# Performance work log

Hardware: AMD Instinct MI355X
Metric: run time of the kernel (lower is better)

## Reference

```python
import jax, jax.numpy as jnp
import numpy as np

B, T, D, H = 64, 512, 256, 512

def setup_inputs() -> dict:
    key = jax.random.key(0)
    ks = jax.random.split(key, 5)
    s = 1.0 / np.sqrt(D + H)  # keep gate pre-activations in a sane range
    return {
        "x": jax.random.normal(ks[0], (B, T, D), dtype=jnp.float32),
        "Wf": jax.random.normal(ks[1], (D + H, H), dtype=jnp.float32) * s,
        "bf": jnp.zeros((H,), dtype=jnp.float32),
        "Wi": jax.random.normal(ks[2], (D + H, H), dtype=jnp.float32) * s,
        "bi": jnp.zeros((H,), dtype=jnp.float32),
        "Wo": jax.random.normal(ks[3], (D + H, H), dtype=jnp.float32) * s,
        "bo": jnp.zeros((H,), dtype=jnp.float32),
        "Wc": jax.random.normal(ks[4], (D + H, H), dtype=jnp.float32) * s,
        "bc": jnp.zeros((H,), dtype=jnp.float32),
    }

def reference(x, Wf, bf, Wi, bi, Wo, bo, Wc, bc):
    # x: [B, T, D]; unidirectional LSTM, zero initial hidden/cell state.
    batch, dur, _ = x.shape
    hid = Wf.shape[1]
    h0 = jnp.zeros((batch, hid), dtype=x.dtype)
    c0 = jnp.zeros((batch, hid), dtype=x.dtype)

    def step(carry, xt):
        h, c = carry
        z = jnp.concatenate([xt, h], axis=1)  # [B, D+H]
        f = jax.nn.sigmoid(z @ Wf + bf)
        i = jax.nn.sigmoid(z @ Wi + bi)
        c_tilde = jnp.tanh(z @ Wc + bc)
        o = jax.nn.sigmoid(z @ Wo + bo)
        c_new = c * f + c_tilde * i
        h_new = o * jnp.tanh(c_new)
        return (h_new, c_new), h_new

    _, hs = jax.lax.scan(step, (h0, c0), jnp.swapaxes(x, 0, 1))  # hs: [T, B, H]
    return jnp.swapaxes(hs, 0, 1)  # [B, T, H]
```

## Files before the change

### kernel.cpp

```cpp
#include <hip/hip_runtime.h>


#define T_   512
#define D_   256
#define H_   512
#define NCL  4
#define WPC  32
#define BPC  16
#define NKT  24
#define ZW   768

typedef __attribute__((ext_vector_type(8)))  short  short8;
typedef __attribute__((ext_vector_type(4)))  float  f32x4;
typedef __attribute__((ext_vector_type(4)))  float  float4_;
typedef unsigned short ushort_t;
typedef unsigned int   uint_t;

__device__ __forceinline__ ushort_t f2bf(float f) {
    unsigned int u = __float_as_uint(f);
    u += 0x7FFFu + ((u >> 16) & 1u);
    return (ushort_t)(u >> 16);
}
__device__ __forceinline__ float sigm_(float x) { return 1.0f / (1.0f + __expf(-x)); }
__device__ __forceinline__ float tanh_(float x) {
    float a = fabsf(x);
    float e = __expf(-2.0f * a);
    float r = (1.0f - e) / (1.0f + e);
    return copysignf(r, x);
}


__device__ __forceinline__ void zbuild_x1(ushort_t* zbuf, int bx, int ch,
                                          float4_ xr0, float4_ xr1,
                                          float4_ xr2, float4_ xr3)
{
    short8 a0, a1;
#pragma unroll
    for (int e = 0; e < 4; ++e) {
        a0[e]     = (short)f2bf(xr0[e]);
        a0[4 + e] = (short)f2bf(xr1[e]);
        a1[e]     = (short)f2bf(xr2[e]);
        a1[4 + e] = (short)f2bf(xr3[e]);
    }
    const int s = bx & 7;
    *(short8*)(zbuf + bx * ZW + (((ch * 2    ) ^ s) << 3)) = a0;
    *(short8*)(zbuf + bx * ZW + (((ch * 2 + 1) ^ s) << 3)) = a1;
}

__global__ __launch_bounds__(256, 1)
void lstm_persistent(const float* __restrict__ x,
                     const float* __restrict__ Wf, const float* __restrict__ bf_,
                     const float* __restrict__ Wi, const float* __restrict__ bi_,
                     const float* __restrict__ Wo, const float* __restrict__ bo_,
                     const float* __restrict__ Wc, const float* __restrict__ bc_,
                     float* __restrict__ out,
                     uint_t* __restrict__ flags,
                     uint_t* __restrict__ hexch)
{
    __shared__ ushort_t w_lds[4 * NKT * 512];
    __shared__ ushort_t z2[2][16 * ZW];
    __shared__ float    gate_lds[4][16][20];
    __shared__ float    bias_lds[64];

    const int tid  = threadIdx.x;
    const int lane = tid & 63;
    const int wv   = tid >> 6;
    const int cl   = blockIdx.x >> 5;
    const int w    = blockIdx.x & 31;
    const int b0   = cl * BPC;
    const int hc0  = w * 16;

    for (int idx = tid; idx < 4 * NKT * 64; idx += 256) {
        int blk   = idx >> 6;
        int ln    = idx & 63;
        int ct    = blk / NKT;
        int kt    = blk % NKT;
        int j     = ct * 16 + (ln & 15);
        int hc    = j >> 2, g = j & 3;
        int gcol  = hc0 + hc;
        const float* Wsrc = (g == 0) ? Wf : ((g == 1) ? Wi : ((g == 2) ? Wo : Wc));
        int krow0 = kt * 32 + (ln >> 4) * 8;
        short8 v;
#pragma unroll
        for (int jj = 0; jj < 8; ++jj)
            v[jj] = (short)f2bf(Wsrc[(size_t)(krow0 + jj) * H_ + gcol]);
        *(short8*)(w_lds + blk * 512 + ln * 8) = v;
    }
    if (tid < 64) {
        int g = tid & 3, hc = tid >> 2;
        const float* bsrc = (g == 0) ? bf_ : ((g == 1) ? bi_ : ((g == 2) ? bo_ : bc_));
        bias_lds[tid] = bsrc[hc0 + hc];
    }

    const int bx = tid & 15, ch = tid >> 4;
    const int l15 = lane & 15, lk = lane >> 4;
    const int hidx = hc0 + wv * 4 + lk;
    const float* xbase = x + (size_t)(b0 + bx) * (T_ * D_) + ch * 16;

    float4_ xr0, xr1, xr2, xr3;
    {
        const float4_* p = (const float4_*)xbase;
        xr0 = p[0]; xr1 = p[1]; xr2 = p[2]; xr3 = p[3];
    }
    zbuild_x1(z2[0], bx, ch, xr0, xr1, xr2, xr3);
    {
        const int zblk0 = 32 + (tid >> 2), zoff2 = (tid & 3) * 2;
#pragma unroll
        for (int r = 0; r < 16; ++r)
            *(uint_t*)(z2[0] + r * ZW + ((zblk0 ^ (r & 7)) << 3) + zoff2) = 0u;
    }
    __syncthreads();

    short8 Bf[NKT];
#pragma unroll
    for (int kt = 0; kt < NKT; ++kt)
        Bf[kt] = *(const short8*)(w_lds + (wv * NKT + kt) * 512 + lane * 8);
    asm volatile("" ::: "memory");

    uint_t* flags_cl = flags + cl * WPC;
    uint_t* hex0 = hexch + ((size_t)0 * NCL + cl) * (BPC * 256);
    uint_t* hex1 = hexch + ((size_t)1 * NCL + cl) * (BPC * 256);

    float c_reg = 0.0f;
    const int s7 = l15 & 7;
    const int blk0 = 32 + (tid >> 2), off2 = (tid & 3) * 2;
    const size_t po = (size_t)l15 * 256 + (hidx >> 1);

    for (int t = 0; t < T_; ++t) {
        const ushort_t* zr = z2[t & 1] + l15 * ZW;
        f32x4 ac0 = {0.f,0.f,0.f,0.f}, ac1 = {0.f,0.f,0.f,0.f};
        f32x4 ac2 = {0.f,0.f,0.f,0.f}, ac3 = {0.f,0.f,0.f,0.f};
#pragma unroll
        for (int kt = 0; kt < NKT; kt += 4) {
            short8 a0 = *(const short8*)(zr + ((((kt + 0) * 4 + lk) ^ s7) << 3));
            short8 a1 = *(const short8*)(zr + ((((kt + 1) * 4 + lk) ^ s7) << 3));
            short8 a2 = *(const short8*)(zr + ((((kt + 2) * 4 + lk) ^ s7) << 3));
            short8 a3 = *(const short8*)(zr + ((((kt + 3) * 4 + lk) ^ s7) << 3));
            ac0 = __builtin_amdgcn_mfma_f32_16x16x32_bf16(a0, Bf[kt + 0], ac0, 0, 0, 0);
            ac1 = __builtin_amdgcn_mfma_f32_16x16x32_bf16(a1, Bf[kt + 1], ac1, 0, 0, 0);
            ac2 = __builtin_amdgcn_mfma_f32_16x16x32_bf16(a2, Bf[kt + 2], ac2, 0, 0, 0);
            ac3 = __builtin_amdgcn_mfma_f32_16x16x32_bf16(a3, Bf[kt + 3], ac3, 0, 0, 0);
        }
        f32x4 acc = (ac0 + ac1) + (ac2 + ac3);

        *(f32x4*)&gate_lds[wv][l15][lk * 4] = acc;
        asm volatile("s_waitcnt lgkmcnt(0)" ::: "memory");
        __builtin_amdgcn_sched_barrier(0);

        float pre[4];
#pragma unroll
        for (int g = 0; g < 4; ++g)
            pre[g] = bias_lds[(wv * 4 + lk) * 4 + g] + gate_lds[wv][lk * 4 + g][l15];

        float fg = sigm_(pre[0]);
        float ig = sigm_(pre[1]);
        float og = sigm_(pre[2]);
        float cc = tanh_(pre[3]);
        c_reg = fmaf(c_reg, fg, cc * ig);
        float hout = og * tanh_(c_reg);

        float hpart = __shfl_xor(hout, 16);
        if (!(lk & 1)) {
            uint_t pk = ((uint_t)f2bf(hpart) << 16) | (uint_t)f2bf(hout);
            uint_t* hp = (((t + 1) & 1) ? hex1 : hex0) + po;
            __hip_atomic_store(hp, pk, __ATOMIC_RELAXED, __HIP_MEMORY_SCOPE_AGENT);
        }

        asm volatile("s_waitcnt vmcnt(0)" ::: "memory");
        __builtin_amdgcn_sched_barrier(0);
        __syncthreads();
        if (tid == 0)
            __hip_atomic_store(flags_cl + w, (uint_t)(t + 1),
                               __ATOMIC_RELAXED, __HIP_MEMORY_SCOPE_AGENT);

        out[((size_t)(b0 + l15) * T_ + t) * H_ + hidx] = hout;
        if (t + 1 < T_) {
            const float4_* p = (const float4_*)(xbase + (size_t)(t + 1) * D_);
            xr0 = p[0]; xr1 = p[1]; xr2 = p[2]; xr3 = p[3];
        }

        if (t + 1 < T_) {
            ushort_t* zn = z2[(t + 1) & 1];

            if (lane < WPC) {
                const uint_t* fp = flags_cl + lane;
                while (__hip_atomic_load(fp, __ATOMIC_RELAXED,
                                         __HIP_MEMORY_SCOPE_AGENT) <= (uint_t)t)
                    __builtin_amdgcn_s_sleep(1);
            }

            const uint_t* hs = (((t + 1) & 1) ? hex1 : hex0);
            uint_t hv[16];
#pragma unroll
            for (int q = 0; q < 16; ++q)
                hv[q] = __hip_atomic_load(hs + q * 256 + tid,
                                          __ATOMIC_RELAXED, __HIP_MEMORY_SCOPE_AGENT);
#pragma unroll
            for (int q = 0; q < 16; ++q)
                *(uint_t*)(zn + q * ZW + ((blk0 ^ (q & 7)) << 3) + off2) = hv[q];

            zbuild_x1(zn, bx, ch, xr0, xr1, xr2, xr3);
        }

        __syncthreads();
    }
}

extern "C" void kernel_launch(void* const* d_in, const int* in_sizes, int n_in,
                              void* d_out, int out_size, void* d_ws, size_t ws_size,
                              hipStream_t stream) {
    const float* x  = (const float*)d_in[0];
    const float* Wf = (const float*)d_in[1];
    const float* bf = (const float*)d_in[2];
    const float* Wi = (const float*)d_in[3];
    const float* bi = (const float*)d_in[4];
    const float* Wo = (const float*)d_in[5];
    const float* bo = (const float*)d_in[6];
    const float* Wc = (const float*)d_in[7];
    const float* bc = (const float*)d_in[8];
    float* out = (float*)d_out;

    uint_t* flags = (uint_t*)d_ws;
    uint_t* hexch = (uint_t*)((char*)d_ws + 4096);

    hipMemsetAsync(d_ws, 0, 4096, stream);

    lstm_persistent<<<dim3(NCL * WPC), dim3(256), 0, stream>>>(
        x, Wf, bf, Wi, bi, Wo, bo, Wc, bc, out, flags, hexch);
}
```

Before: 1.553 ms.

## Regroup LSTM workgroups into 8 clusters of 8 batches with 32 hidden units each

```diff
diff --git a/kernel.cpp b/kernel.cpp
--- a/kernel.cpp
+++ b/kernel.cpp
@@ -4,9 +4,9 @@
 #define T_   512
 #define D_   256
 #define H_   512
-#define NCL  4
-#define WPC  32
-#define BPC  16
+#define NCL  8
+#define WPC  16
+#define BPC  8
 #define NKT  24
 #define ZW   768
 
@@ -29,23 +29,6 @@
     return copysignf(r, x);
 }
 
-
-__device__ __forceinline__ void zbuild_x1(ushort_t* zbuf, int bx, int ch,
-                                          float4_ xr0, float4_ xr1,
-                                          float4_ xr2, float4_ xr3)
-{
-    short8 a0, a1;
-#pragma unroll
-    for (int e = 0; e < 4; ++e) {
-        a0[e]     = (short)f2bf(xr0[e]);
-        a0[4 + e] = (short)f2bf(xr1[e]);
-        a1[e]     = (short)f2bf(xr2[e]);
-        a1[4 + e] = (short)f2bf(xr3[e]);
-    }
-    const int s = bx & 7;
-    *(short8*)(zbuf + bx * ZW + (((ch * 2    ) ^ s) << 3)) = a0;
-    *(short8*)(zbuf + bx * ZW + (((ch * 2 + 1) ^ s) << 3)) = a1;
-}
 
 __global__ __launch_bounds__(256, 1)
 void lstm_persistent(const float* __restrict__ x,
@@ -59,63 +42,79 @@
 {
     __shared__ ushort_t w_lds[4 * NKT * 512];
     __shared__ ushort_t z2[2][16 * ZW];
-    __shared__ float    gate_lds[4][16][20];
-    __shared__ float    bias_lds[64];
+    __shared__ float    gate_lds[4][2][16][12];
+    __shared__ float    bias_lds[128];
 
     const int tid  = threadIdx.x;
     const int lane = tid & 63;
     const int wv   = tid >> 6;
-    const int cl   = blockIdx.x >> 5;
-    const int w    = blockIdx.x & 31;
+    const int cl   = blockIdx.x >> 4;
+    const int w    = blockIdx.x & 15;
     const int b0   = cl * BPC;
-    const int hc0  = w * 16;
-
-    for (int idx = tid; idx < 4 * NKT * 64; idx += 256) {
-        int blk   = idx >> 6;
-        int ln    = idx & 63;
-        int ct    = blk / NKT;
-        int kt    = blk % NKT;
-        int j     = ct * 16 + (ln & 15);
-        int hc    = j >> 2, g = j & 3;
-        int gcol  = hc0 + hc;
-        const float* Wsrc = (g == 0) ? Wf : ((g == 1) ? Wi : ((g == 2) ? Wo : Wc));
-        int krow0 = kt * 32 + (ln >> 4) * 8;
-        short8 v;
-#pragma unroll
-        for (int jj = 0; jj < 8; ++jj)
-            v[jj] = (short)f2bf(Wsrc[(size_t)(krow0 + jj) * H_ + gcol]);
-        *(short8*)(w_lds + blk * 512 + ln * 8) = v;
-    }
-    if (tid < 64) {
+    const int hc0  = w * 32;
+
+    {
+        uint_t* zz = (uint_t*)z2;
+        for (int i = tid; i < 2 * 16 * ZW / 2; i += 256) zz[i] = 0;
+    }
+
+#define REPACK(CT_BASE)                                                        \
+    for (int idx = tid; idx < 4 * NKT * 64; idx += 256) {                      \
+        int blk   = idx >> 6;                                       \
+        int ln    = idx & 63;                                                  \
+        int ct    = (CT_BASE) + blk / NKT;                                     \
+        int kt    = blk % NKT;                                                 \
+        int j     = ct * 16 + (ln & 15);                  \
+        int hc    = j >> 2, g = j & 3;                                         \
+        int gcol  = hc0 + hc;                                                  \
+        const float* Wsrc = (g == 0) ? Wf : ((g == 1) ? Wi                     \
+                            : ((g == 2) ? Wo : Wc));                           \
+        int krow0 = kt * 32 + (ln >> 4) * 8;                                   \
+        short8 v;                                                              \
+        _Pragma("unroll")                                                      \
+        for (int jj = 0; jj < 8; ++jj)                                         \
+            v[jj] = (short)f2bf(Wsrc[(size_t)(krow0 + jj) * H_ + gcol]);       \
+        *(short8*)(w_lds + blk * 512 + ln * 8) = v;                            \
+    }
+    REPACK(4)
+    __syncthreads();
+
+    short8 Bf[NKT];
+#pragma unroll
+    for (int kt = 0; kt < NKT; ++kt)
+        Bf[kt] = *(const short8*)(w_lds + (wv * NKT + kt) * 512 + lane * 8);
+    asm volatile("" ::: "memory");
+    __syncthreads();
+
+    REPACK(0)
+#undef REPACK
+    if (tid < 128) {
         int g = tid & 3, hc = tid >> 2;
         const float* bsrc = (g == 0) ? bf_ : ((g == 1) ? bi_ : ((g == 2) ? bo_ : bc_));
         bias_lds[tid] = bsrc[hc0 + hc];
     }
 
-    const int bx = tid & 15, ch = tid >> 4;
+    const int bx = tid & 7, ch = tid >> 3;
     const int l15 = lane & 15, lk = lane >> 4;
-    const int hidx = hc0 + wv * 4 + lk;
-    const float* xbase = x + (size_t)(b0 + bx) * (T_ * D_) + ch * 16;
-
-    float4_ xr0, xr1, xr2, xr3;
+    const int gb   = lane >> 3;
+    const int hsel = lane & 7;
+    const int hcl  = (hsel < 4) ? (wv * 4 + hsel) : (16 + wv * 4 + (hsel - 4));
+    const int gtile = hsel >> 2;
+    const int gcol4 = (hsel & 3) * 4;
+    const float* xbase = x + (size_t)(b0 + bx) * (T_ * D_) + ch * 8;
+
     {
         const float4_* p = (const float4_*)xbase;
-        xr0 = p[0]; xr1 = p[1]; xr2 = p[2]; xr3 = p[3];
-    }
-    zbuild_x1(z2[0], bx, ch, xr0, xr1, xr2, xr3);
-    {
-        const int zblk0 = 32 + (tid >> 2), zoff2 = (tid & 3) * 2;
-#pragma unroll
-        for (int r = 0; r < 16; ++r)
-            *(uint_t*)(z2[0] + r * ZW + ((zblk0 ^ (r & 7)) << 3) + zoff2) = 0u;
+        float4_ x0 = p[0], x1 = p[1];
+        short8 a;
+#pragma unroll
+        for (int e = 0; e < 4; ++e) {
+            a[e]     = (short)f2bf(x0[e]);
+            a[4 + e] = (short)f2bf(x1[e]);
+        }
+        *(short8*)(z2[0] + bx * ZW + ((ch ^ (bx & 7)) << 3)) = a;
     }
     __syncthreads();
-
-    short8 Bf[NKT];
-#pragma unroll
-    for (int kt = 0; kt < NKT; ++kt)
-        Bf[kt] = *(const short8*)(w_lds + (wv * NKT + kt) * 512 + lane * 8);
-    asm volatile("" ::: "memory");
 
     uint_t* flags_cl = flags + cl * WPC;
     uint_t* hex0 = hexch + ((size_t)0 * NCL + cl) * (BPC * 256);
@@ -124,33 +123,39 @@
     float c_reg = 0.0f;
     const int s7 = l15 & 7;
     const int blk0 = 32 + (tid >> 2), off2 = (tid & 3) * 2;
-    const size_t po = (size_t)l15 * 256 + (hidx >> 1);
+    const size_t po = (size_t)gb * 256 + ((hc0 + hcl) >> 1);
+    const ushort_t* wl = w_lds + (wv * NKT) * 512 + lane * 8;
+    float4_ xq0, xq1;
 
     for (int t = 0; t < T_; ++t) {
         const ushort_t* zr = z2[t & 1] + l15 * ZW;
-        f32x4 ac0 = {0.f,0.f,0.f,0.f}, ac1 = {0.f,0.f,0.f,0.f};
-        f32x4 ac2 = {0.f,0.f,0.f,0.f}, ac3 = {0.f,0.f,0.f,0.f};
-#pragma unroll
-        for (int kt = 0; kt < NKT; kt += 4) {
-            short8 a0 = *(const short8*)(zr + ((((kt + 0) * 4 + lk) ^ s7) << 3));
-            short8 a1 = *(const short8*)(zr + ((((kt + 1) * 4 + lk) ^ s7) << 3));
-            short8 a2 = *(const short8*)(zr + ((((kt + 2) * 4 + lk) ^ s7) << 3));
-            short8 a3 = *(const short8*)(zr + ((((kt + 3) * 4 + lk) ^ s7) << 3));
-            ac0 = __builtin_amdgcn_mfma_f32_16x16x32_bf16(a0, Bf[kt + 0], ac0, 0, 0, 0);
-            ac1 = __builtin_amdgcn_mfma_f32_16x16x32_bf16(a1, Bf[kt + 1], ac1, 0, 0, 0);
-            ac2 = __builtin_amdgcn_mfma_f32_16x16x32_bf16(a2, Bf[kt + 2], ac2, 0, 0, 0);
-            ac3 = __builtin_amdgcn_mfma_f32_16x16x32_bf16(a3, Bf[kt + 3], ac3, 0, 0, 0);
-        }
-        f32x4 acc = (ac0 + ac1) + (ac2 + ac3);
-
-        *(f32x4*)&gate_lds[wv][l15][lk * 4] = acc;
+        f32x4 aL0 = {0.f,0.f,0.f,0.f}, aL1 = {0.f,0.f,0.f,0.f};
+        f32x4 aV0 = {0.f,0.f,0.f,0.f}, aV1 = {0.f,0.f,0.f,0.f};
+#pragma unroll
+        for (int kt = 0; kt < NKT; kt += 2) {
+            short8 a0  = *(const short8*)(zr + ((((kt + 0) * 4 + lk) ^ s7) << 3));
+            short8 a1  = *(const short8*)(zr + ((((kt + 1) * 4 + lk) ^ s7) << 3));
+            short8 bl0 = *(const short8*)(wl + (kt + 0) * 512);
+            short8 bl1 = *(const short8*)(wl + (kt + 1) * 512);
+            aL0 = __builtin_amdgcn_mfma_f32_16x16x32_bf16(a0, bl0,        aL0, 0, 0, 0);
+            aV0 = __builtin_amdgcn_mfma_f32_16x16x32_bf16(a0, Bf[kt + 0], aV0, 0, 0, 0);
+            aL1 = __builtin_amdgcn_mfma_f32_16x16x32_bf16(a1, bl1,        aL1, 0, 0, 0);
+            aV1 = __builtin_amdgcn_mfma_f32_16x16x32_bf16(a1, Bf[kt + 1], aV1, 0, 0, 0);
+        }
+        f32x4 accL = aL0 + aL1;
+        f32x4 accV = aV0 + aV1;
+
+        if (lk < 2) {
+            *(f32x4*)&gate_lds[wv][0][l15][lk * 4] = accL;
+            *(f32x4*)&gate_lds[wv][1][l15][lk * 4] = accV;
+        }
         asm volatile("s_waitcnt lgkmcnt(0)" ::: "memory");
         __builtin_amdgcn_sched_barrier(0);
 
         float pre[4];
 #pragma unroll
         for (int g = 0; g < 4; ++g)
-            pre[g] = bias_lds[(wv * 4 + lk) * 4 + g] + gate_lds[wv][lk * 4 + g][l15];
+            pre[g] = bias_lds[hcl * 4 + g] + gate_lds[wv][gtile][gcol4 + g][gb];
 
         float fg = sigm_(pre[0]);
         float ig = sigm_(pre[1]);
@@ -159,8 +164,8 @@
         c_reg = fmaf(c_reg, fg, cc * ig);
         float hout = og * tanh_(c_reg);
 
-        float hpart = __shfl_xor(hout, 16);
-        if (!(lk & 1)) {
+        float hpart = __shfl_xor(hout, 1);
+        if (!(hsel & 1)) {
             uint_t pk = ((uint_t)f2bf(hpart) << 16) | (uint_t)f2bf(hout);
             uint_t* hp = (((t + 1) & 1) ? hex1 : hex0) + po;
             __hip_atomic_store(hp, pk, __ATOMIC_RELAXED, __HIP_MEMORY_SCOPE_AGENT);
@@ -173,10 +178,10 @@
             __hip_atomic_store(flags_cl + w, (uint_t)(t + 1),
                                __ATOMIC_RELAXED, __HIP_MEMORY_SCOPE_AGENT);
 
-        out[((size_t)(b0 + l15) * T_ + t) * H_ + hidx] = hout;
+        out[((size_t)(b0 + gb) * T_ + t) * H_ + hc0 + hcl] = hout;
         if (t + 1 < T_) {
             const float4_* p = (const float4_*)(xbase + (size_t)(t + 1) * D_);
-            xr0 = p[0]; xr1 = p[1]; xr2 = p[2]; xr3 = p[3];
+            xq0 = p[0]; xq1 = p[1];
         }
 
         if (t + 1 < T_) {
@@ -190,16 +195,24 @@
             }
 
             const uint_t* hs = (((t + 1) & 1) ? hex1 : hex0);
-            uint_t hv[16];
-#pragma unroll
-            for (int q = 0; q < 16; ++q)
-                hv[q] = __hip_atomic_load(hs + q * 256 + tid,
+            uint_t hv[8];
+#pragma unroll
+            for (int b = 0; b < 8; ++b)
+                hv[b] = __hip_atomic_load(hs + b * 256 + tid,
                                           __ATOMIC_RELAXED, __HIP_MEMORY_SCOPE_AGENT);
 #pragma unroll
-            for (int q = 0; q < 16; ++q)
-                *(uint_t*)(zn + q * ZW + ((blk0 ^ (q & 7)) << 3) + off2) = hv[q];
-
-            zbuild_x1(zn, bx, ch, xr0, xr1, xr2, xr3);
+            for (int b = 0; b < 8; ++b)
+                *(uint_t*)(zn + b * ZW + ((blk0 ^ b) << 3) + off2) = hv[b];
+
+            {
+                short8 a;
+#pragma unroll
+                for (int e = 0; e < 4; ++e) {
+                    a[e]     = (short)f2bf(xq0[e]);
+                    a[4 + e] = (short)f2bf(xq1[e]);
+                }
+                *(short8*)(zn + bx * ZW + ((ch ^ (bx & 7)) << 3)) = a;
+            }
         }
 
         __syncthreads();
```

Measured after the change: 1.912 ms. +23.1%, slower.
